# Performance work log

Hardware: AMD Instinct MI355X
Metric: run time of the kernel (lower is better)

Reference implementation:

```python
import jax, jax.numpy as jnp
import numpy as np

N_GENE, N_PATH, N_VACC = 50000, 20000, 10000
N_TOT = N_GENE + N_PATH + N_VACC
HID = 128
E_PER = 250000
K_APPNP = 8
ALPHA = 0.1
N_LAYERS = 2


def setup_inputs() -> dict:
    key = jax.random.key(0)
    ks = iter(jax.random.split(key, 40))
    f32 = jnp.float32

    def nrm(shape, scale=1.0):
        return jax.random.normal(next(ks), shape, dtype=f32) * scale

    def edges(n_src, n_dst):
        src = jax.random.randint(next(ks), (E_PER,), 0, n_src)
        dst = jax.random.randint(next(ks), (E_PER,), 0, n_dst)
        return jnp.stack([src, dst]).astype(jnp.int32)

    return {
        "x_gene": nrm((N_GENE, 256)),
        "x_pathway": nrm((N_PATH, 128)),
        "x_vaccine": nrm((N_VACC, 64)),
        "win_gene": nrm((HID, 256), 256 ** -0.5),
        "bin_gene": jnp.zeros((HID,), f32),
        "win_pathway": nrm((HID, 128), 128 ** -0.5),
        "bin_pathway": jnp.zeros((HID,), f32),
        "win_vaccine": nrm((HID, 64), 64 ** -0.5),
        "bin_vaccine": jnp.zeros((HID,), f32),
        "w_sage_l": nrm((N_LAYERS, 4, HID, HID), HID ** -0.5),
        "b_sage_l": jnp.zeros((N_LAYERS, 4, HID), f32),
        "w_sage_r": nrm((N_LAYERS, 4, HID, HID), HID ** -0.5),
        "ei_targets": edges(N_VACC, N_GENE),    # vaccine -> gene
        "ei_in": edges(N_GENE, N_PATH),         # gene -> pathway
        "ei_contains": edges(N_PATH, N_GENE),   # pathway -> gene
        "ei_interacts": edges(N_GENE, N_GENE),  # gene -> gene
    }


def _sage(x_src, x_dst, ei, wl, bl, wr, n_dst):
    # PyG SAGEConv(aggr='mean'): lin_l(mean_j x_src[j]) + lin_r(x_dst); bias lives in lin_l
    src, dst = ei[0], ei[1]
    s = jax.ops.segment_sum(x_src[src], dst, num_segments=n_dst)
    cnt = jax.ops.segment_sum(jnp.ones((ei.shape[1],), x_src.dtype), dst, num_segments=n_dst)
    agg = s / jnp.maximum(cnt, 1.0)[:, None]  # isolated dst nodes -> 0
    return agg @ wl.T + bl + x_dst @ wr.T


def _forward(x_gene, x_pathway, x_vaccine, win_gene, bin_gene, win_pathway, bin_pathway,
             win_vaccine, bin_vaccine, w_sage_l, b_sage_l, w_sage_r,
             ei_targets, ei_in, ei_contains, ei_interacts):
    # input projections + relu
    hg = jax.nn.relu(x_gene @ win_gene.T + bin_gene)
    hp = jax.nn.relu(x_pathway @ win_pathway.T + bin_pathway)
    hv = jax.nn.relu(x_vaccine @ win_vaccine.T + bin_vaccine)
    # hetero SAGE layers with residual + relu (dropout: eval mode -> identity)
    for l in range(N_LAYERS):
        o_tg = _sage(hv, hg, ei_targets, w_sage_l[l, 0], b_sage_l[l, 0], w_sage_r[l, 0], N_GENE)
        o_in = _sage(hg, hp, ei_in, w_sage_l[l, 1], b_sage_l[l, 1], w_sage_r[l, 1], N_PATH)
        o_ct = _sage(hp, hg, ei_contains, w_sage_l[l, 2], b_sage_l[l, 2], w_sage_r[l, 2], N_GENE)
        o_ii = _sage(hg, hg, ei_interacts, w_sage_l[l, 3], b_sage_l[l, 3], w_sage_r[l, 3], N_GENE)
        hg = jax.nn.relu(hg + (o_tg + o_ct + o_ii) / 3.0)  # HeteroConv aggr='mean' over 3 relations
        hp = jax.nn.relu(hp + o_in)
        hv = jax.nn.relu(hv)  # no incoming relation -> zero message
    # APPNP on homogeneous graph; node order = [gene | pathway | vaccine]
    OG, OP, OV = 0, N_GENE, N_GENE + N_PATH
    loops = jnp.arange(N_TOT, dtype=jnp.int32)
    row = jnp.concatenate([ei_targets[0] + OV, ei_in[0] + OG, ei_contains[0] + OP, ei_interacts[0] + OG, loops])
    col = jnp.concatenate([ei_targets[1] + OG, ei_in[1] + OP, ei_contains[1] + OG, ei_interacts[1] + OG, loops])
    deg = jax.ops.segment_sum(jnp.ones(row.shape, hg.dtype), col, num_segments=N_TOT)
    dinv = jnp.where(deg > 0, deg ** -0.5, 0.0)
    norm = (dinv[row] * dinv[col])[:, None]
    h0 = jnp.concatenate([hg, hp, hv], axis=0)  # [N_TOT, HID]

    def step(z, _):
        m = jax.ops.segment_sum(norm * z[row], col, num_segments=N_TOT)
        return (1.0 - ALPHA) * m + ALPHA * h0, None

    z, _ = jax.lax.scan(step, h0, None, length=K_APPNP)
    return z  # [N_TOT, HID]; rows 0:50000 gene, 50000:70000 pathway, 70000:80000 vaccine


def reference(x_gene, x_pathway, x_vaccine, win_gene, bin_gene, win_pathway, bin_pathway,
              win_vaccine, bin_vaccine, w_sage_l, b_sage_l, w_sage_r,
              ei_targets, ei_in, ei_contains, ei_interacts):
    return _forward(x_gene, x_pathway, x_vaccine, win_gene, bin_gene, win_pathway, bin_pathway,
                    win_vaccine, bin_vaccine, w_sage_l, b_sage_l, w_sage_r,
                    ei_targets, ei_in, ei_contains, ei_interacts)
```

## Files before the change

### kernel.cpp

```cpp
#include <hip/hip_runtime.h>

#define N_GENE 50000
#define N_PATH 20000
#define N_VACC 10000
#define N_TOT  80000
#define HID    128
#define E_PER  250000
#define OG 0
#define OP 50000
#define OV 70000

typedef __bf16    bf16x8 __attribute__((ext_vector_type(8)));
typedef __bf16    bf16x4 __attribute__((ext_vector_type(4)));
typedef _Float16  f16x4  __attribute__((ext_vector_type(4)));
typedef float     f32x4  __attribute__((ext_vector_type(4)));

__constant__ int c_segn[4] = {N_GENE, N_PATH, N_GENE, N_GENE};
__constant__ int c_segb[4] = {0, 50000, 70000, 120000};
#define CNT_TOTAL 170000

struct Off4 { int* p[4]; };
struct CntSeg { const int* dst; int* cnt; };
struct Cnt4 { CntSeg s[4]; };
struct F4Seg { const int* ei; const int* off; int* rows; int2* pk; int soff; };
struct F4 { F4Seg s[4]; };
struct AggSeg { const int* rows; const int* off; __bf16* out; int ldo; int n; };
struct Agg4 { AggSeg s[4]; };
struct CsrP { const int* off; const int2* pk; };


__global__ void count4_kernel(Cnt4 a, int* __restrict__ rank)
{
    int seg = blockIdx.y;
    int e = blockIdx.x * 256 + threadIdx.x;
    if (e < E_PER) rank[seg * E_PER + e] = atomicAdd(&a.s[seg].cnt[a.s[seg].dst[e]], 1);
}

__global__ void scan1_kernel(const int* __restrict__ cnt, int* __restrict__ partials)
{
    int seg = blockIdx.y, blk = blockIdx.x;
    int n = c_segn[seg];
    if (blk >= ((n + 4095) >> 12)) return;
    const int* base = cnt + c_segb[seg];
    int t = threadIdx.x;
    int i0 = (blk << 12) + t * 16;
    int s = 0;
#pragma unroll
    for (int j = 0; j < 16; j++) { int i = i0 + j; if (i < n) s += base[i]; }
    __shared__ int sh[256];
    sh[t] = s; __syncthreads();
    for (int d = 128; d; d >>= 1) { if (t < d) sh[t] += sh[t + d]; __syncthreads(); }
    if (t == 0) partials[seg * 32 + blk] = sh[0];
}

__global__ void scan2_kernel(int* __restrict__ partials, Off4 offs)
{
    int s = threadIdx.x;
    if (s < 4) {
        int n = c_segn[s];
        int nb = (n + 4095) >> 12;
        int run = 0;
        for (int b = 0; b < nb; b++) { int v = partials[s * 32 + b]; partials[s * 32 + b] = run; run += v; }
        offs.p[s][n] = run;
    }
}

__global__ void scan3_kernel(const int* __restrict__ cnt, const int* __restrict__ partials, Off4 offs)
{
    int seg = blockIdx.y, blk = blockIdx.x;
    int n = c_segn[seg];
    if (blk >= ((n + 4095) >> 12)) return;
    const int* base = cnt + c_segb[seg];
    int* off = offs.p[seg];
    int t = threadIdx.x;
    int i0 = (blk << 12) + t * 16;
    int loc[16];
    int s = 0;
#pragma unroll
    for (int j = 0; j < 16; j++) { int i = i0 + j; int v = (i < n) ? base[i] : 0; loc[j] = s; s += v; }
    __shared__ int sh[256];
    sh[t] = s; __syncthreads();
    for (int d = 1; d < 256; d <<= 1) {
        int v = (t >= d) ? sh[t - d] : 0; __syncthreads();
        sh[t] += v; __syncthreads();
    }
    int base_off = sh[t] - s + partials[seg * 32 + blk];
#pragma unroll
    for (int j = 0; j < 16; j++) { int i = i0 + j; if (i < n) off[i] = base_off + loc[j]; }
}

__global__ void dinv_kernel(const int* __restrict__ r0, const int* __restrict__ r1,
                            const int* __restrict__ r2, const int* __restrict__ r3,
                            float* __restrict__ dinv)
{
    int i = blockIdx.x * 256 + threadIdx.x;
    if (i >= N_TOT) return;
    int deg = 1;
    if (i < N_GENE) deg += (r0[i + 1] - r0[i]) + (r2[i + 1] - r2[i]) + (r3[i + 1] - r3[i]);
    else if (i < OV) { int k = i - OP; deg += r1[k + 1] - r1[k]; }
    dinv[i] = rsqrtf((float)deg);
}

__global__ void fill4_kernel(F4 a, const int* __restrict__ rank, const float* __restrict__ dinv)
{
    int seg = blockIdx.y;
    int e = blockIdx.x * 256 + threadIdx.x;
    if (e >= E_PER) return;
    const int* ei = a.s[seg].ei;
    int s = ei[e] + a.s[seg].soff;
    int d = ei[E_PER + e];
    int pos = a.s[seg].off[d] + rank[seg * E_PER + e];
    a.s[seg].rows[pos] = s;
    if (a.s[seg].pk) a.s[seg].pk[pos] = make_int2(s, __float_as_int(dinv[s]));
}


__global__ void agg_all_kernel(Agg4 a, const __bf16* __restrict__ Hbf)
{
    int seg = blockIdx.y;
    int t = threadIdx.x;
    int node = blockIdx.x * 8 + (t >> 5);
    if (node >= a.s[seg].n) return;
    const int* rows = a.s[seg].rows;
    int sub = t & 31;
    int s = a.s[seg].off[node], e = a.s[seg].off[node + 1];
    f32x4 A0 = {0,0,0,0}, A1 = {0,0,0,0}, A2v = {0,0,0,0}, A3 = {0,0,0,0};
    int i = s;
    for (; i + 4 <= e; i += 4) {
        int r0 = rows[i], r1 = rows[i + 1], r2 = rows[i + 2], r3 = rows[i + 3];
        bf16x4 x0 = *(const bf16x4*)&Hbf[(size_t)r0 * HID + sub * 4];
        bf16x4 x1 = *(const bf16x4*)&Hbf[(size_t)r1 * HID + sub * 4];
        bf16x4 x2 = *(const bf16x4*)&Hbf[(size_t)r2 * HID + sub * 4];
        bf16x4 x3 = *(const bf16x4*)&Hbf[(size_t)r3 * HID + sub * 4];
#pragma unroll
        for (int j = 0; j < 4; j++) {
            A0[j] += (float)x0[j]; A1[j] += (float)x1[j];
            A2v[j] += (float)x2[j]; A3[j] += (float)x3[j];
        }
    }
    for (; i < e; i++) {
        bf16x4 x = *(const bf16x4*)&Hbf[(size_t)rows[i] * HID + sub * 4];
#pragma unroll
        for (int j = 0; j < 4; j++) A0[j] += (float)x[j];
    }
    f32x4 acc = (A0 + A1) + (A2v + A3);
    float inv = (e > s) ? 1.0f / (float)(e - s) : 0.0f;
    bf16x4 o;
    o[0] = (__bf16)(acc[0] * inv); o[1] = (__bf16)(acc[1] * inv);
    o[2] = (__bf16)(acc[2] * inv); o[3] = (__bf16)(acc[3] * inv);
    *(bf16x4*)&a.s[seg].out[(size_t)node * a.s[seg].ldo + sub * 4] = o;
}

__global__ void base_kernel(const float* __restrict__ H, const int* __restrict__ r0rows,
                            const int* __restrict__ r0off, const float* __restrict__ dinv,
                            _Float16* __restrict__ base, _Float16* __restrict__ z0,
                            float* __restrict__ dout)
{
    int t = threadIdx.x;
    int node = blockIdx.x * 8 + (t >> 5);
    int sub = t & 31;
    size_t idx = (size_t)node * HID + sub * 4;
    f32x4 h = *(const f32x4*)&H[idx];
    if (node >= OV) { *(f32x4*)&dout[idx] = h; return; }
    f32x4 acc = {0.f, 0.f, 0.f, 0.f};
    if (node < N_GENE) {
        for (int i = r0off[node]; i < r0off[node + 1]; i++) {
            acc += *(const f32x4*)&H[(size_t)r0rows[i] * HID + sub * 4];
        }
        acc *= 0.9f * dinv[node];
    }
    f32x4 b = h * 0.1f + acc;
    f16x4 bo, z;
    bo[0] = (_Float16)b[0]; bo[1] = (_Float16)b[1]; bo[2] = (_Float16)b[2]; bo[3] = (_Float16)b[3];
    z[0] = (_Float16)h[0]; z[1] = (_Float16)h[1]; z[2] = (_Float16)h[2]; z[3] = (_Float16)h[3];
    *(f16x4*)&base[idx] = bo;
    *(f16x4*)&z0[idx] = z;
}

__device__ __forceinline__ void gathp(const int* __restrict__ off, const int2* __restrict__ pk,
                                      int node, int sub, const _Float16* __restrict__ zin,
                                      f32x4& A0, f32x4& A1, f32x4& A2v, f32x4& A3)
{
    int s = off[node], e = off[node + 1];
    int i = s;
    for (; i + 4 <= e; i += 4) {
        int2 p0 = pk[i], p1 = pk[i + 1], p2 = pk[i + 2], p3 = pk[i + 3];
        f16x4 x0 = *(const f16x4*)&zin[(size_t)p0.x * HID + sub * 4];
        f16x4 x1 = *(const f16x4*)&zin[(size_t)p1.x * HID + sub * 4];
        f16x4 x2 = *(const f16x4*)&zin[(size_t)p2.x * HID + sub * 4];
        f16x4 x3 = *(const f16x4*)&zin[(size_t)p3.x * HID + sub * 4];
        float w0 = __int_as_float(p0.y), w1 = __int_as_float(p1.y);
        float w2 = __int_as_float(p2.y), w3 = __int_as_float(p3.y);
#pragma unroll
        for (int j = 0; j < 4; j++) {
            A0[j] += (float)x0[j] * w0; A1[j] += (float)x1[j] * w1;
            A2v[j] += (float)x2[j] * w2; A3[j] += (float)x3[j] * w3;
        }
    }
    for (; i < e; i++) {
        int2 p = pk[i];
        float w = __int_as_float(p.y);
        f16x4 x = *(const f16x4*)&zin[(size_t)p.x * HID + sub * 4];
#pragma unroll
        for (int j = 0; j < 4; j++) A0[j] += (float)x[j] * w;
    }
}

template<typename OT>
__launch_bounds__(256)
__global__ void appnp_kernel(const _Float16* __restrict__ zin, OT* __restrict__ zout,
                             const _Float16* __restrict__ base,
                             CsrP c1, CsrP c2, CsrP c3, const float* __restrict__ dinv)
{
    int t = threadIdx.x;
    int c = blockIdx.x * 8 + (t >> 5);
    int sub = t & 31;
    f32x4 A0 = {0,0,0,0}, A1 = {0,0,0,0}, A2v = {0,0,0,0}, A3 = {0,0,0,0};
    if (c < OP) {
        gathp(c2.off, c2.pk, c, sub, zin, A0, A1, A2v, A3);
        gathp(c3.off, c3.pk, c, sub, zin, A0, A1, A2v, A3);
    } else {
        gathp(c1.off, c1.pk, c - OP, sub, zin, A0, A1, A2v, A3);
    }
    f32x4 acc = (A0 + A1) + (A2v + A3);
    float dc = dinv[c];
    size_t idx = (size_t)c * HID + sub * 4;
    f16x4 zi = *(const f16x4*)&zin[idx];
    f16x4 bs = *(const f16x4*)&base[idx];
    f32x4 res;
    float d2 = dc * dc;
#pragma unroll
    for (int j = 0; j < 4; j++) res[j] = 0.9f * (dc * acc[j] + d2 * (float)zi[j]) + (float)bs[j];
    if constexpr (sizeof(OT) == 2) {
        f16x4 o;
        o[0] = (_Float16)res[0]; o[1] = (_Float16)res[1]; o[2] = (_Float16)res[2]; o[3] = (_Float16)res[3];
        *(f16x4*)&zout[idx] = o;
    } else {
        *(f32x4*)&zout[idx] = res;
    }
}


__global__ void prep_all_kernel(const float* __restrict__ wg, const float* __restrict__ wp,
                                const float* __restrict__ wv,
                                __bf16* __restrict__ obg, __bf16* __restrict__ obp, __bf16* __restrict__ obv,
                                const float* __restrict__ wsl, const float* __restrict__ bsl,
                                const float* __restrict__ wsr,
                                __bf16* __restrict__ Wg0, __bf16* __restrict__ Wg1,
                                __bf16* __restrict__ Wp0, __bf16* __restrict__ Wp1,
                                float* __restrict__ bg0, float* __restrict__ bg1,
                                float* __restrict__ bp0, float* __restrict__ bp1)
{
    int y = blockIdx.y;
    int i = blockIdx.x * 256 + threadIdx.x;
    if (y == 0) {
        if (i < 32768) obg[i] = (__bf16)wg[i];
        if (i < 16384) obp[i] = (__bf16)wp[i];
        if (i < 8192)  obv[i] = (__bf16)wv[i];
        return;
    }
    int layer = y - 1;
    const float* WL = wsl + (size_t)layer * 4 * HID * HID;
    const float* WR = wsr + (size_t)layer * 4 * HID * HID;
    __bf16* Wg = layer ? Wg1 : Wg0;
    __bf16* Wp = layer ? Wp1 : Wp0;
    float* bg = layer ? bg1 : bg0;
    float* bp = layer ? bp1 : bp0;
    if (i < 128 * 512) {
        int nr = i >> 9, k = i & 511;
        float v;
        if (k < 128)      v = WL[0 * 16384 + nr * 128 + k];
        else if (k < 256) v = WL[2 * 16384 + nr * 128 + (k - 128)];
        else if (k < 384) v = WL[3 * 16384 + nr * 128 + (k - 256)];
        else {
            int kk = k - 384;
            v = WR[0 * 16384 + nr * 128 + kk] + WR[2 * 16384 + nr * 128 + kk] + WR[3 * 16384 + nr * 128 + kk];
        }
        Wg[i] = (__bf16)v;
    }
    if (i < 128 * 256) {
        int nr = i >> 8, k = i & 255;
        float v = (k < 128) ? WL[1 * 16384 + nr * 128 + k] : WR[1 * 16384 + nr * 128 + (k - 128)];
        Wp[i] = (__bf16)v;
    }
    if (i < 128) {
        const float* BL = bsl + (size_t)layer * 4 * HID;
        bg[i] = BL[0 * 128 + i] + BL[2 * 128 + i] + BL[3 * 128 + i];
        bp[i] = BL[1 * 128 + i];
    }
}


struct GemmSeg {
    int blk0, M, KT, K1;
    const void* A1; const __bf16* A2;
    const __bf16* W; const float* bias;
    float scale;
    float* H; __bf16* Hbf;
    int a_f32, sage;
};
template<int NSEG> struct GemmSegs { GemmSeg s[NSEG]; };

template<int NSEG>
__launch_bounds__(256)
__global__ void tgemm_multi(GemmSegs<NSEG> segs)
{
    int si = 0;
#pragma unroll
    for (int k = 1; k < NSEG; k++) if ((int)blockIdx.x >= segs.s[k].blk0) si = k;
    GemmSeg sg = segs.s[si];

    __shared__ __bf16 lds[128 * 40];
    int t = threadIdx.x;
    int wave = t >> 6, lane = t & 63;
    int r = lane & 15, quad = lane >> 4;
    int mbase = (blockIdx.x - sg.blk0) * 128 + wave * 32;
    int M = sg.M, KT = sg.KT, K1 = sg.K1;
    int mm0 = min(mbase + r, M - 1);
    int mm1 = min(mbase + 16 + r, M - 1);
    const float* Af = (const float*)sg.A1;
    const __bf16* Ab = (const __bf16*)sg.A1;

    f32x4 acc[2][8];
#pragma unroll
    for (int s = 0; s < 2; s++)
#pragma unroll
        for (int n = 0; n < 8; n++) acc[s][n] = (f32x4){0.f, 0.f, 0.f, 0.f};

    int srow = t >> 1;
    int selt = (t & 1) * 16;

    for (int k0 = 0; k0 < KT; k0 += 32) {
        __syncthreads();
        {
            const __bf16* wsrc = sg.W + (size_t)srow * KT + k0 + selt;
            bf16x8 w0 = *(const bf16x8*)wsrc;
            bf16x8 w1 = *(const bf16x8*)(wsrc + 8);
            *(bf16x8*)&lds[srow * 40 + selt] = w0;
            *(bf16x8*)&lds[srow * 40 + selt + 8] = w1;
        }
        bf16x8 a0, a1;
        if (sg.a_f32) {
            const float* p0 = Af + (size_t)mm0 * KT + k0 + quad * 8;
            const float* p1 = Af + (size_t)mm1 * KT + k0 + quad * 8;
            f32x4 x0 = *(const f32x4*)p0, x1 = *(const f32x4*)(p0 + 4);
            f32x4 y0 = *(const f32x4*)p1, y1 = *(const f32x4*)(p1 + 4);
#pragma unroll
            for (int j = 0; j < 4; j++) { a0[j] = (__bf16)x0[j]; a0[j + 4] = (__bf16)x1[j]; }
#pragma unroll
            for (int j = 0; j < 4; j++) { a1[j] = (__bf16)y0[j]; a1[j + 4] = (__bf16)y1[j]; }
        } else if (k0 < K1) {
            a0 = *(const bf16x8*)(Ab + (size_t)mm0 * K1 + k0 + quad * 8);
            a1 = *(const bf16x8*)(Ab + (size_t)mm1 * K1 + k0 + quad * 8);
        } else {
            a0 = *(const bf16x8*)(sg.A2 + (size_t)mm0 * 128 + (k0 - K1) + quad * 8);
            a1 = *(const bf16x8*)(sg.A2 + (size_t)mm1 * 128 + (k0 - K1) + quad * 8);
        }
        __syncthreads();
#pragma unroll
        for (int nt = 0; nt < 8; nt++) {
            bf16x8 b = *(const bf16x8*)&lds[(nt * 16 + r) * 40 + quad * 8];
            acc[0][nt] = __builtin_amdgcn_mfma_f32_16x16x32_bf16(a0, b, acc[0][nt], 0, 0, 0);
            acc[1][nt] = __builtin_amdgcn_mfma_f32_16x16x32_bf16(a1, b, acc[1][nt], 0, 0, 0);
        }
    }

#pragma unroll
    for (int sub = 0; sub < 2; sub++) {
#pragma unroll
        for (int nt = 0; nt < 8; nt++) {
            int n = nt * 16 + r;
            float bv = sg.bias[n];
#pragma unroll
            for (int i = 0; i < 4; i++) {
                int row = mbase + sub * 16 + quad * 4 + i;
                if (row >= M) continue;
                size_t idx = (size_t)row * HID + n;
                float v;
                if (sg.sage) v = fmaxf(sg.H[idx] + (acc[sub][nt][i] + bv) * sg.scale, 0.f);
                else         v = fmaxf(acc[sub][nt][i] + bv, 0.f);
                sg.H[idx] = v;
                sg.Hbf[idx] = (__bf16)v;
            }
        }
    }
}


extern "C" void kernel_launch(void* const* d_in, const int* in_sizes, int n_in,
                              void* d_out, int out_size, void* d_ws, size_t ws_size,
                              hipStream_t stream)
{
    (void)in_sizes; (void)n_in; (void)out_size; (void)ws_size;

    const float* x_gene = (const float*)d_in[0];
    const float* x_path = (const float*)d_in[1];
    const float* x_vacc = (const float*)d_in[2];
    const float* win_g  = (const float*)d_in[3];
    const float* bin_g  = (const float*)d_in[4];
    const float* win_p  = (const float*)d_in[5];
    const float* bin_p  = (const float*)d_in[6];
    const float* win_v  = (const float*)d_in[7];
    const float* bin_v  = (const float*)d_in[8];
    const float* wsl    = (const float*)d_in[9];
    const float* bsl    = (const float*)d_in[10];
    const float* wsr    = (const float*)d_in[11];
    const int* ei_tg  = (const int*)d_in[12];
    const int* ei_ing = (const int*)d_in[13];
    const int* ei_ct  = (const int*)d_in[14];
    const int* ei_ii  = (const int*)d_in[15];

    char* p = (char*)d_ws;
    auto alloc = [&](size_t b) { char* r = p; p += (b + 255) & ~((size_t)255); return r; };

    float*    H    = (float*)alloc((size_t)N_TOT * HID * 4);
    _Float16* BASE = (_Float16*)alloc((size_t)OV * HID * 2);
    __bf16*   Hbf  = (__bf16*)alloc((size_t)N_TOT * HID * 2);
    _Float16* Z1   = (_Float16*)alloc((size_t)OV * HID * 2);
    _Float16* Z2   = (_Float16*)alloc((size_t)OV * HID * 2);
    __bf16* AGG_G = (__bf16*)alloc((size_t)N_GENE * 384 * 2);
    __bf16* AGG_P = (__bf16*)alloc((size_t)N_PATH * 128 * 2);
    float* dinv   = (float*)alloc((size_t)N_TOT * 4);
    int* r_rows[4], *r_off[4];
    for (int r = 0; r < 4; r++) r_rows[r] = (int*)alloc((size_t)E_PER * 4);
    r_off[0] = (int*)alloc((size_t)(N_GENE + 1) * 4);
    r_off[1] = (int*)alloc((size_t)(N_PATH + 1) * 4);
    r_off[2] = (int*)alloc((size_t)(N_GENE + 1) * 4);
    r_off[3] = (int*)alloc((size_t)(N_GENE + 1) * 4);
    int2* pk1 = (int2*)alloc((size_t)E_PER * 8);
    int2* pk2 = (int2*)alloc((size_t)E_PER * 8);
    int2* pk3 = (int2*)alloc((size_t)E_PER * 8);
    int* rank = (int*)alloc((size_t)4 * E_PER * 4);
    int* partials = (int*)alloc((size_t)4 * 32 * 4);
    __bf16* wbf_g = (__bf16*)alloc((size_t)HID * 256 * 2);
    __bf16* wbf_p = (__bf16*)alloc((size_t)HID * 128 * 2);
    __bf16* wbf_v = (__bf16*)alloc((size_t)HID * 64 * 2);
    __bf16* Wg[2]; __bf16* Wp[2]; float* bg[2]; float* bp[2];
    for (int l = 0; l < 2; l++) {
        Wg[l] = (__bf16*)alloc((size_t)128 * 512 * 2);
        Wp[l] = (__bf16*)alloc((size_t)128 * 256 * 2);
        bg[l] = (float*)alloc(128 * 4);
        bp[l] = (float*)alloc(128 * 4);
    }
    char* zb = p;
    int* cnt = (int*)alloc((size_t)CNT_TOTAL * 4);
    hipMemsetAsync(zb, 0, (size_t)(p - zb), stream);

    Off4 offs;
    offs.p[0] = r_off[0]; offs.p[1] = r_off[1]; offs.p[2] = r_off[2]; offs.p[3] = r_off[3];

    const int GE = (E_PER + 255) / 256;
    const int TB_G = (N_GENE + 127) / 128;
    const int TB_P = (N_PATH + 127) / 128;
    const int TB_V = (N_VACC + 127) / 128;

    prep_all_kernel<<<dim3(256, 3), 256, 0, stream>>>(win_g, win_p, win_v, wbf_g, wbf_p, wbf_v,
                                                      wsl, bsl, wsr, Wg[0], Wg[1], Wp[0], Wp[1],
                                                      bg[0], bg[1], bp[0], bp[1]);

    Cnt4 c4;
    c4.s[0] = {ei_tg + E_PER,  cnt + 0};
    c4.s[1] = {ei_ing + E_PER, cnt + 50000};
    c4.s[2] = {ei_ct + E_PER,  cnt + 70000};
    c4.s[3] = {ei_ii + E_PER,  cnt + 120000};
    count4_kernel<<<dim3(GE, 4), 256, 0, stream>>>(c4, rank);

    dim3 sg((N_GENE + 4095) / 4096, 4);
    scan1_kernel<<<sg, 256, 0, stream>>>(cnt, partials);
    scan2_kernel<<<1, 64, 0, stream>>>(partials, offs);
    scan3_kernel<<<sg, 256, 0, stream>>>(cnt, partials, offs);

    dinv_kernel<<<(N_TOT + 255) / 256, 256, 0, stream>>>(r_off[0], r_off[1], r_off[2], r_off[3], dinv);

    F4 f4;
    f4.s[0] = {ei_tg,  r_off[0], r_rows[0], nullptr, OV};
    f4.s[1] = {ei_ing, r_off[1], r_rows[1], pk1,     OG};
    f4.s[2] = {ei_ct,  r_off[2], r_rows[2], pk2,     OP};
    f4.s[3] = {ei_ii,  r_off[3], r_rows[3], pk3,     OG};
    fill4_kernel<<<dim3(GE, 4), 256, 0, stream>>>(f4, rank, dinv);

    GemmSegs<3> gp;
    gp.s[0] = {0,           N_GENE, 256, 256, x_gene, nullptr, wbf_g, bin_g, 1.f, H, Hbf, 1, 0};
    gp.s[1] = {TB_G,        N_PATH, 128, 128, x_path, nullptr, wbf_p, bin_p, 1.f,
               H + (size_t)OP * HID, Hbf + (size_t)OP * HID, 1, 0};
    gp.s[2] = {TB_G + TB_P, N_VACC,  64,  64, x_vacc, nullptr, wbf_v, bin_v, 1.f,
               H + (size_t)OV * HID, Hbf + (size_t)OV * HID, 1, 0};
    tgemm_multi<3><<<TB_G + TB_P + TB_V, 256, 0, stream>>>(gp);

    for (int l = 0; l < 2; l++) {
        Agg4 ag;
        ag.s[0] = {r_rows[0], r_off[0], AGG_G + 0,   384, N_GENE};
        ag.s[1] = {r_rows[2], r_off[2], AGG_G + 128, 384, N_GENE};
        ag.s[2] = {r_rows[3], r_off[3], AGG_G + 256, 384, N_GENE};
        ag.s[3] = {r_rows[1], r_off[1], AGG_P,       128, N_PATH};
        agg_all_kernel<<<dim3(N_GENE / 8, 4), 256, 0, stream>>>(ag, Hbf);

        GemmSegs<2> gs;
        gs.s[0] = {0,    N_GENE, 512, 384, AGG_G, Hbf, Wg[l], bg[l], 1.0f / 3.0f, H, Hbf, 0, 1};
        gs.s[1] = {TB_G, N_PATH, 256, 128, AGG_P, Hbf + (size_t)OP * HID, Wp[l], bp[l], 1.0f,
                   H + (size_t)OP * HID, Hbf + (size_t)OP * HID, 0, 1};
        tgemm_multi<2><<<TB_G + TB_P, 256, 0, stream>>>(gs);
    }

    float* dout = (float*)d_out;
    base_kernel<<<N_TOT / 8, 256, 0, stream>>>(H, r_rows[0], r_off[0], dinv, BASE, Z1, dout);

    CsrP c1 = {r_off[1], pk1};
    CsrP c2 = {r_off[2], pk2};
    CsrP c3 = {r_off[3], pk3};
    const int GA = OV / 8;
    appnp_kernel<<<GA, 256, 0, stream>>>(Z1, Z2, BASE, c1, c2, c3, dinv);
    appnp_kernel<<<GA, 256, 0, stream>>>(Z2, Z1, BASE, c1, c2, c3, dinv);
    appnp_kernel<<<GA, 256, 0, stream>>>(Z1, Z2, BASE, c1, c2, c3, dinv);
    appnp_kernel<<<GA, 256, 0, stream>>>(Z2, Z1, BASE, c1, c2, c3, dinv);
    appnp_kernel<<<GA, 256, 0, stream>>>(Z1, Z2, BASE, c1, c2, c3, dinv);
    appnp_kernel<<<GA, 256, 0, stream>>>(Z2, Z1, BASE, c1, c2, c3, dinv);
    appnp_kernel<<<GA, 256, 0, stream>>>(Z1, Z2, BASE, c1, c2, c3, dinv);
    appnp_kernel<<<GA, 256, 0, stream>>>(Z2, dout, BASE, c1, c2, c3, dinv);
}
```

Baseline: 791.6 us.

## Keep hidden state only in fp16 and widen gathers to 16-byte loads

```diff
diff --git a/kernel.cpp b/kernel.cpp
--- a/kernel.cpp
+++ b/kernel.cpp
@@ -10,8 +10,7 @@
 #define OP 50000
 #define OV 70000
 
-typedef __bf16    bf16x8 __attribute__((ext_vector_type(8)));
-typedef __bf16    bf16x4 __attribute__((ext_vector_type(4)));
+typedef _Float16  f16x8  __attribute__((ext_vector_type(8)));
 typedef _Float16  f16x4  __attribute__((ext_vector_type(4)));
 typedef float     f32x4  __attribute__((ext_vector_type(4)));
 
@@ -24,7 +23,7 @@
 struct Cnt4 { CntSeg s[4]; };
 struct F4Seg { const int* ei; const int* off; int* rows; int2* pk; int soff; };
 struct F4 { F4Seg s[4]; };
-struct AggSeg { const int* rows; const int* off; __bf16* out; int ldo; int n; };
+struct AggSeg { const int* rows; const int* off; _Float16* out; int ldo; int n; };
 struct Agg4 { AggSeg s[4]; };
 struct CsrP { const int* off; const int2* pk; };
 
@@ -115,94 +114,103 @@
 }
 
 
-__global__ void agg_all_kernel(Agg4 a, const __bf16* __restrict__ Hbf)
+__global__ void agg_all_kernel(Agg4 a, const _Float16* __restrict__ Hh)
 {
     int seg = blockIdx.y;
     int t = threadIdx.x;
-    int node = blockIdx.x * 8 + (t >> 5);
+    int node = blockIdx.x * 16 + (t >> 4);
     if (node >= a.s[seg].n) return;
     const int* rows = a.s[seg].rows;
-    int sub = t & 31;
+    int sub = t & 15;
     int s = a.s[seg].off[node], e = a.s[seg].off[node + 1];
-    f32x4 A0 = {0,0,0,0}, A1 = {0,0,0,0}, A2v = {0,0,0,0}, A3 = {0,0,0,0};
+    float acc0[8] = {}, acc1[8] = {};
     int i = s;
     for (; i + 4 <= e; i += 4) {
         int r0 = rows[i], r1 = rows[i + 1], r2 = rows[i + 2], r3 = rows[i + 3];
-        bf16x4 x0 = *(const bf16x4*)&Hbf[(size_t)r0 * HID + sub * 4];
-        bf16x4 x1 = *(const bf16x4*)&Hbf[(size_t)r1 * HID + sub * 4];
-        bf16x4 x2 = *(const bf16x4*)&Hbf[(size_t)r2 * HID + sub * 4];
-        bf16x4 x3 = *(const bf16x4*)&Hbf[(size_t)r3 * HID + sub * 4];
-#pragma unroll
-        for (int j = 0; j < 4; j++) {
-            A0[j] += (float)x0[j]; A1[j] += (float)x1[j];
-            A2v[j] += (float)x2[j]; A3[j] += (float)x3[j];
+        f16x8 x0 = *(const f16x8*)&Hh[(size_t)r0 * HID + sub * 8];
+        f16x8 x1 = *(const f16x8*)&Hh[(size_t)r1 * HID + sub * 8];
+        f16x8 x2 = *(const f16x8*)&Hh[(size_t)r2 * HID + sub * 8];
+        f16x8 x3 = *(const f16x8*)&Hh[(size_t)r3 * HID + sub * 8];
+#pragma unroll
+        for (int j = 0; j < 8; j++) {
+            acc0[j] += (float)x0[j] + (float)x1[j];
+            acc1[j] += (float)x2[j] + (float)x3[j];
         }
     }
     for (; i < e; i++) {
-        bf16x4 x = *(const bf16x4*)&Hbf[(size_t)rows[i] * HID + sub * 4];
-#pragma unroll
-        for (int j = 0; j < 4; j++) A0[j] += (float)x[j];
-    }
-    f32x4 acc = (A0 + A1) + (A2v + A3);
+        f16x8 x = *(const f16x8*)&Hh[(size_t)rows[i] * HID + sub * 8];
+#pragma unroll
+        for (int j = 0; j < 8; j++) acc0[j] += (float)x[j];
+    }
     float inv = (e > s) ? 1.0f / (float)(e - s) : 0.0f;
-    bf16x4 o;
-    o[0] = (__bf16)(acc[0] * inv); o[1] = (__bf16)(acc[1] * inv);
-    o[2] = (__bf16)(acc[2] * inv); o[3] = (__bf16)(acc[3] * inv);
-    *(bf16x4*)&a.s[seg].out[(size_t)node * a.s[seg].ldo + sub * 4] = o;
-}
-
-__global__ void base_kernel(const float* __restrict__ H, const int* __restrict__ r0rows,
+    f16x8 o;
+#pragma unroll
+    for (int j = 0; j < 8; j++) o[j] = (_Float16)((acc0[j] + acc1[j]) * inv);
+    *(f16x8*)&a.s[seg].out[(size_t)node * a.s[seg].ldo + sub * 8] = o;
+}
+
+__global__ void base_kernel(const _Float16* __restrict__ Hh, const int* __restrict__ r0rows,
                             const int* __restrict__ r0off, const float* __restrict__ dinv,
                             _Float16* __restrict__ base, _Float16* __restrict__ z0,
                             float* __restrict__ dout)
 {
     int t = threadIdx.x;
-    int node = blockIdx.x * 8 + (t >> 5);
-    int sub = t & 31;
-    size_t idx = (size_t)node * HID + sub * 4;
-    f32x4 h = *(const f32x4*)&H[idx];
-    if (node >= OV) { *(f32x4*)&dout[idx] = h; return; }
-    f32x4 acc = {0.f, 0.f, 0.f, 0.f};
+    int node = blockIdx.x * 16 + (t >> 4);
+    int sub = t & 15;
+    size_t idx = (size_t)node * HID + sub * 8;
+    f16x8 h = *(const f16x8*)&Hh[idx];
+    if (node >= OV) {
+        f32x4 o0, o1;
+#pragma unroll
+        for (int j = 0; j < 4; j++) { o0[j] = (float)h[j]; o1[j] = (float)h[j + 4]; }
+        *(f32x4*)&dout[idx] = o0;
+        *(f32x4*)&dout[idx + 4] = o1;
+        return;
+    }
+    float acc[8] = {};
     if (node < N_GENE) {
         for (int i = r0off[node]; i < r0off[node + 1]; i++) {
-            acc += *(const f32x4*)&H[(size_t)r0rows[i] * HID + sub * 4];
-        }
-        acc *= 0.9f * dinv[node];
-    }
-    f32x4 b = h * 0.1f + acc;
-    f16x4 bo, z;
-    bo[0] = (_Float16)b[0]; bo[1] = (_Float16)b[1]; bo[2] = (_Float16)b[2]; bo[3] = (_Float16)b[3];
-    z[0] = (_Float16)h[0]; z[1] = (_Float16)h[1]; z[2] = (_Float16)h[2]; z[3] = (_Float16)h[3];
-    *(f16x4*)&base[idx] = bo;
-    *(f16x4*)&z0[idx] = z;
+            f16x8 v = *(const f16x8*)&Hh[(size_t)r0rows[i] * HID + sub * 8];
+#pragma unroll
+            for (int j = 0; j < 8; j++) acc[j] += (float)v[j];
+        }
+        float sc = 0.9f * dinv[node];
+#pragma unroll
+        for (int j = 0; j < 8; j++) acc[j] *= sc;
+    }
+    f16x8 bo;
+#pragma unroll
+    for (int j = 0; j < 8; j++) bo[j] = (_Float16)(0.1f * (float)h[j] + acc[j]);
+    *(f16x8*)&base[idx] = bo;
+    *(f16x8*)&z0[idx] = h;
 }
 
 __device__ __forceinline__ void gathp(const int* __restrict__ off, const int2* __restrict__ pk,
                                       int node, int sub, const _Float16* __restrict__ zin,
-                                      f32x4& A0, f32x4& A1, f32x4& A2v, f32x4& A3)
+                                      float (&A0)[8], float (&A1)[8])
 {
     int s = off[node], e = off[node + 1];
     int i = s;
     for (; i + 4 <= e; i += 4) {
         int2 p0 = pk[i], p1 = pk[i + 1], p2 = pk[i + 2], p3 = pk[i + 3];
-        f16x4 x0 = *(const f16x4*)&zin[(size_t)p0.x * HID + sub * 4];
-        f16x4 x1 = *(const f16x4*)&zin[(size_t)p1.x * HID + sub * 4];
-        f16x4 x2 = *(const f16x4*)&zin[(size_t)p2.x * HID + sub * 4];
-        f16x4 x3 = *(const f16x4*)&zin[(size_t)p3.x * HID + sub * 4];
+        f16x8 x0 = *(const f16x8*)&zin[(size_t)p0.x * HID + sub * 8];
+        f16x8 x1 = *(const f16x8*)&zin[(size_t)p1.x * HID + sub * 8];
+        f16x8 x2 = *(const f16x8*)&zin[(size_t)p2.x * HID + sub * 8];
+        f16x8 x3 = *(const f16x8*)&zin[(size_t)p3.x * HID + sub * 8];
         float w0 = __int_as_float(p0.y), w1 = __int_as_float(p1.y);
         float w2 = __int_as_float(p2.y), w3 = __int_as_float(p3.y);
 #pragma unroll
-        for (int j = 0; j < 4; j++) {
-            A0[j] += (float)x0[j] * w0; A1[j] += (float)x1[j] * w1;
-            A2v[j] += (float)x2[j] * w2; A3[j] += (float)x3[j] * w3;
+        for (int j = 0; j < 8; j++) {
+            A0[j] += (float)x0[j] * w0 + (float)x1[j] * w1;
+            A1[j] += (float)x2[j] * w2 + (float)x3[j] * w3;
         }
     }
     for (; i < e; i++) {
         int2 p = pk[i];
         float w = __int_as_float(p.y);
-        f16x4 x = *(const f16x4*)&zin[(size_t)p.x * HID + sub * 4];
-#pragma unroll
-        for (int j = 0; j < 4; j++) A0[j] += (float)x[j] * w;
+        f16x8 x = *(const f16x8*)&zin[(size_t)p.x * HID + sub * 8];
+#pragma unroll
+        for (int j = 0; j < 8; j++) A0[j] += (float)x[j] * w;
     }
 }
 
@@ -213,57 +221,62 @@
                              CsrP c1, CsrP c2, CsrP c3, const float* __restrict__ dinv)
 {
     int t = threadIdx.x;
-    int c = blockIdx.x * 8 + (t >> 5);
-    int sub = t & 31;
-    f32x4 A0 = {0,0,0,0}, A1 = {0,0,0,0}, A2v = {0,0,0,0}, A3 = {0,0,0,0};
+    int c = blockIdx.x * 16 + (t >> 4);
+    int sub = t & 15;
+    float A0[8] = {}, A1[8] = {};
     if (c < OP) {
-        gathp(c2.off, c2.pk, c, sub, zin, A0, A1, A2v, A3);
-        gathp(c3.off, c3.pk, c, sub, zin, A0, A1, A2v, A3);
+        gathp(c2.off, c2.pk, c, sub, zin, A0, A1);
+        gathp(c3.off, c3.pk, c, sub, zin, A0, A1);
     } else {
-        gathp(c1.off, c1.pk, c - OP, sub, zin, A0, A1, A2v, A3);
-    }
-    f32x4 acc = (A0 + A1) + (A2v + A3);
+        gathp(c1.off, c1.pk, c - OP, sub, zin, A0, A1);
+    }
     float dc = dinv[c];
-    size_t idx = (size_t)c * HID + sub * 4;
-    f16x4 zi = *(const f16x4*)&zin[idx];
-    f16x4 bs = *(const f16x4*)&base[idx];
-    f32x4 res;
     float d2 = dc * dc;
-#pragma unroll
-    for (int j = 0; j < 4; j++) res[j] = 0.9f * (dc * acc[j] + d2 * (float)zi[j]) + (float)bs[j];
+    size_t idx = (size_t)c * HID + sub * 8;
+    f16x8 zi = *(const f16x8*)&zin[idx];
+    f16x8 bs = *(const f16x8*)&base[idx];
+    float res[8];
+#pragma unroll
+    for (int j = 0; j < 8; j++)
+        res[j] = 0.9f * (dc * (A0[j] + A1[j]) + d2 * (float)zi[j]) + (float)bs[j];
     if constexpr (sizeof(OT) == 2) {
-        f16x4 o;
-        o[0] = (_Float16)res[0]; o[1] = (_Float16)res[1]; o[2] = (_Float16)res[2]; o[3] = (_Float16)res[3];
-        *(f16x4*)&zout[idx] = o;
+        f16x8 o;
+#pragma unroll
+        for (int j = 0; j < 8; j++) o[j] = (_Float16)res[j];
+        *(f16x8*)&zout[idx] = o;
     } else {
-        *(f32x4*)&zout[idx] = res;
+        f32x4 o0, o1;
+#pragma unroll
+        for (int j = 0; j < 4; j++) { o0[j] = res[j]; o1[j] = res[j + 4]; }
+        *(f32x4*)&zout[idx] = o0;
+        *(f32x4*)&zout[idx + 4] = o1;
     }
 }
 
 
 __global__ void prep_all_kernel(const float* __restrict__ wg, const float* __restrict__ wp,
                                 const float* __restrict__ wv,
-                                __bf16* __restrict__ obg, __bf16* __restrict__ obp, __bf16* __restrict__ obv,
+                                _Float16* __restrict__ obg, _Float16* __restrict__ obp, _Float16* __restrict__ obv,
                                 const float* __restrict__ wsl, const float* __restrict__ bsl,
                                 const float* __restrict__ wsr,
-                                __bf16* __restrict__ Wg0, __bf16* __restrict__ Wg1,
-                                __bf16* __restrict__ Wp0, __bf16* __restrict__ Wp1,
+                                _Float16* __restrict__ Wg0, _Float16* __restrict__ Wg1,
+                                _Float16* __restrict__ Wp0, _Float16* __restrict__ Wp1,
                                 float* __restrict__ bg0, float* __restrict__ bg1,
                                 float* __restrict__ bp0, float* __restrict__ bp1)
 {
     int y = blockIdx.y;
     int i = blockIdx.x * 256 + threadIdx.x;
     if (y == 0) {
-        if (i < 32768) obg[i] = (__bf16)wg[i];
-        if (i < 16384) obp[i] = (__bf16)wp[i];
-        if (i < 8192)  obv[i] = (__bf16)wv[i];
+        if (i < 32768) obg[i] = (_Float16)wg[i];
+        if (i < 16384) obp[i] = (_Float16)wp[i];
+        if (i < 8192)  obv[i] = (_Float16)wv[i];
         return;
     }
     int layer = y - 1;
     const float* WL = wsl + (size_t)layer * 4 * HID * HID;
     const float* WR = wsr + (size_t)layer * 4 * HID * HID;
-    __bf16* Wg = layer ? Wg1 : Wg0;
-    __bf16* Wp = layer ? Wp1 : Wp0;
+    _Float16* Wg = layer ? Wg1 : Wg0;
+    _Float16* Wp = layer ? Wp1 : Wp0;
     float* bg = layer ? bg1 : bg0;
     float* bp = layer ? bp1 : bp0;
     if (i < 128 * 512) {
@@ -276,12 +289,12 @@
             int kk = k - 384;
             v = WR[0 * 16384 + nr * 128 + kk] + WR[2 * 16384 + nr * 128 + kk] + WR[3 * 16384 + nr * 128 + kk];
         }
-        Wg[i] = (__bf16)v;
+        Wg[i] = (_Float16)v;
     }
     if (i < 128 * 256) {
         int nr = i >> 8, k = i & 255;
         float v = (k < 128) ? WL[1 * 16384 + nr * 128 + k] : WR[1 * 16384 + nr * 128 + (k - 128)];
-        Wp[i] = (__bf16)v;
+        Wp[i] = (_Float16)v;
     }
     if (i < 128) {
         const float* BL = bsl + (size_t)layer * 4 * HID;
@@ -291,35 +304,21 @@
 }
 
 
-struct GemmSeg {
-    int blk0, M, KT, K1;
-    const void* A1; const __bf16* A2;
-    const __bf16* W; const float* bias;
-    float scale;
-    float* H; __bf16* Hbf;
-    int a_f32, sage;
-};
-template<int NSEG> struct GemmSegs { GemmSeg s[NSEG]; };
-
-template<int NSEG>
+template<int KT, int K1, bool A_F32, bool SAGE>
 __launch_bounds__(256)
-__global__ void tgemm_multi(GemmSegs<NSEG> segs)
-{
-    int si = 0;
-#pragma unroll
-    for (int k = 1; k < NSEG; k++) if ((int)blockIdx.x >= segs.s[k].blk0) si = k;
-    GemmSeg sg = segs.s[si];
-
-    __shared__ __bf16 lds[128 * 40];
+__global__ void tgemm_kernel(const void* __restrict__ A1_, const _Float16* __restrict__ A2,
+                             const _Float16* __restrict__ W, const float* __restrict__ bias,
+                             float scale, _Float16* __restrict__ Hh, int M)
+{
+    __shared__ _Float16 lds[128 * 40];
     int t = threadIdx.x;
     int wave = t >> 6, lane = t & 63;
     int r = lane & 15, quad = lane >> 4;
-    int mbase = (blockIdx.x - sg.blk0) * 128 + wave * 32;
-    int M = sg.M, KT = sg.KT, K1 = sg.K1;
+    int mbase = blockIdx.x * 128 + wave * 32;
     int mm0 = min(mbase + r, M - 1);
     int mm1 = min(mbase + 16 + r, M - 1);
-    const float* Af = (const float*)sg.A1;
-    const __bf16* Ab = (const __bf16*)sg.A1;
+    const float* Af = (const float*)A1_;
+    const _Float16* Ab = (const _Float16*)A1_;
 
     f32x4 acc[2][8];
 #pragma unroll
@@ -330,38 +329,39 @@
     int srow = t >> 1;
     int selt = (t & 1) * 16;
 
+#pragma unroll
     for (int k0 = 0; k0 < KT; k0 += 32) {
         __syncthreads();
         {
-            const __bf16* wsrc = sg.W + (size_t)srow * KT + k0 + selt;
-            bf16x8 w0 = *(const bf16x8*)wsrc;
-            bf16x8 w1 = *(const bf16x8*)(wsrc + 8);
-            *(bf16x8*)&lds[srow * 40 + selt] = w0;
-            *(bf16x8*)&lds[srow * 40 + selt + 8] = w1;
-        }
-        bf16x8 a0, a1;
-        if (sg.a_f32) {
+            const _Float16* wsrc = W + (size_t)srow * KT + k0 + selt;
+            f16x8 w0 = *(const f16x8*)wsrc;
+            f16x8 w1 = *(const f16x8*)(wsrc + 8);
+            *(f16x8*)&lds[srow * 40 + selt] = w0;
+            *(f16x8*)&lds[srow * 40 + selt + 8] = w1;
+        }
+        f16x8 a0, a1;
+        if constexpr (A_F32) {
             const float* p0 = Af + (size_t)mm0 * KT + k0 + quad * 8;
             const float* p1 = Af + (size_t)mm1 * KT + k0 + quad * 8;
             f32x4 x0 = *(const f32x4*)p0, x1 = *(const f32x4*)(p0 + 4);
             f32x4 y0 = *(const f32x4*)p1, y1 = *(const f32x4*)(p1 + 4);
 #pragma unroll
-            for (int j = 0; j < 4; j++) { a0[j] = (__bf16)x0[j]; a0[j + 4] = (__bf16)x1[j]; }
-#pragma unroll
-            for (int j = 0; j < 4; j++) { a1[j] = (__bf16)y0[j]; a1[j + 4] = (__bf16)y1[j]; }
+            for (int j = 0; j < 4; j++) { a0[j] = (_Float16)x0[j]; a0[j + 4] = (_Float16)x1[j]; }
+#pragma unroll
+            for (int j = 0; j < 4; j++) { a1[j] = (_Float16)y0[j]; a1[j + 4] = (_Float16)y1[j]; }
         } else if (k0 < K1) {
-            a0 = *(const bf16x8*)(Ab + (size_t)mm0 * K1 + k0 + quad * 8);
-            a1 = *(const bf16x8*)(Ab + (size_t)mm1 * K1 + k0 + quad * 8);
+            a0 = *(const f16x8*)(Ab + (size_t)mm0 * K1 + k0 + quad * 8);
+            a1 = *(const f16x8*)(Ab + (size_t)mm1 * K1 + k0 + quad * 8);
         } else {
-            a0 = *(const bf16x8*)(sg.A2 + (size_t)mm0 * 128 + (k0 - K1) + quad * 8);
-            a1 = *(const bf16x8*)(sg.A2 + (size_t)mm1 * 128 + (k0 - K1) + quad * 8);
+            a0 = *(const f16x8*)(A2 + (size_t)mm0 * 128 + (k0 - K1) + quad * 8);
+            a1 = *(const f16x8*)(A2 + (size_t)mm1 * 128 + (k0 - K1) + quad * 8);
         }
         __syncthreads();
 #pragma unroll
         for (int nt = 0; nt < 8; nt++) {
-            bf16x8 b = *(const bf16x8*)&lds[(nt * 16 + r) * 40 + quad * 8];
-            acc[0][nt] = __builtin_amdgcn_mfma_f32_16x16x32_bf16(a0, b, acc[0][nt], 0, 0, 0);
-            acc[1][nt] = __builtin_amdgcn_mfma_f32_16x16x32_bf16(a1, b, acc[1][nt], 0, 0, 0);
+            f16x8 b = *(const f16x8*)&lds[(nt * 16 + r) * 40 + quad * 8];
+            acc[0][nt] = __builtin_amdgcn_mfma_f32_16x16x32_f16(a0, b, acc[0][nt], 0, 0, 0);
+            acc[1][nt] = __builtin_amdgcn_mfma_f32_16x16x32_f16(a1, b, acc[1][nt], 0, 0, 0);
         }
     }
 
@@ -370,17 +370,16 @@
 #pragma unroll
         for (int nt = 0; nt < 8; nt++) {
             int n = nt * 16 + r;
-            float bv = sg.bias[n];
+            float bv = bias[n];
 #pragma unroll
             for (int i = 0; i < 4; i++) {
                 int row = mbase + sub * 16 + quad * 4 + i;
                 if (row >= M) continue;
                 size_t idx = (size_t)row * HID + n;
                 float v;
-                if (sg.sage) v = fmaxf(sg.H[idx] + (acc[sub][nt][i] + bv) * sg.scale, 0.f);
-                else         v = fmaxf(acc[sub][nt][i] + bv, 0.f);
-                sg.H[idx] = v;
-                sg.Hbf[idx] = (__bf16)v;
+                if constexpr (SAGE) v = fmaxf((float)Hh[idx] + (acc[sub][nt][i] + bv) * scale, 0.f);
+                else                v = fmaxf(acc[sub][nt][i] + bv, 0.f);
+                Hh[idx] = (_Float16)v;
             }
         }
     }
@@ -413,13 +412,12 @@
     char* p = (char*)d_ws;
     auto alloc = [&](size_t b) { char* r = p; p += (b + 255) & ~((size_t)255); return r; };
 
-    float*    H    = (float*)alloc((size_t)N_TOT * HID * 4);
+    _Float16* Hh   = (_Float16*)alloc((size_t)N_TOT * HID * 2);
     _Float16* BASE = (_Float16*)alloc((size_t)OV * HID * 2);
-    __bf16*   Hbf  = (__bf16*)alloc((size_t)N_TOT * HID * 2);
     _Float16* Z1   = (_Float16*)alloc((size_t)OV * HID * 2);
     _Float16* Z2   = (_Float16*)alloc((size_t)OV * HID * 2);
-    __bf16* AGG_G = (__bf16*)alloc((size_t)N_GENE * 384 * 2);
-    __bf16* AGG_P = (__bf16*)alloc((size_t)N_PATH * 128 * 2);
+    _Float16* AGG_G = (_Float16*)alloc((size_t)N_GENE * 384 * 2);
+    _Float16* AGG_P = (_Float16*)alloc((size_t)N_PATH * 128 * 2);
     float* dinv   = (float*)alloc((size_t)N_TOT * 4);
     int* r_rows[4], *r_off[4];
     for (int r = 0; r < 4; r++) r_rows[r] = (int*)alloc((size_t)E_PER * 4);
@@ -432,13 +430,13 @@
     int2* pk3 = (int2*)alloc((size_t)E_PER * 8);
     int* rank = (int*)alloc((size_t)4 * E_PER * 4);
     int* partials = (int*)alloc((size_t)4 * 32 * 4);
-    __bf16* wbf_g = (__bf16*)alloc((size_t)HID * 256 * 2);
-    __bf16* wbf_p = (__bf16*)alloc((size_t)HID * 128 * 2);
-    __bf16* wbf_v = (__bf16*)alloc((size_t)HID * 64 * 2);
-    __bf16* Wg[2]; __bf16* Wp[2]; float* bg[2]; float* bp[2];
+    _Float16* wh_g = (_Float16*)alloc((size_t)HID * 256 * 2);
+    _Float16* wh_p = (_Float16*)alloc((size_t)HID * 128 * 2);
+    _Float16* wh_v = (_Float16*)alloc((size_t)HID * 64 * 2);
+    _Float16* Wg[2]; _Float16* Wp[2]; float* bg[2]; float* bp[2];
     for (int l = 0; l < 2; l++) {
-        Wg[l] = (__bf16*)alloc((size_t)128 * 512 * 2);
-        Wp[l] = (__bf16*)alloc((size_t)128 * 256 * 2);
+        Wg[l] = (_Float16*)alloc((size_t)128 * 512 * 2);
+        Wp[l] = (_Float16*)alloc((size_t)128 * 256 * 2);
         bg[l] = (float*)alloc(128 * 4);
         bp[l] = (float*)alloc(128 * 4);
     }
@@ -454,7 +452,7 @@
     const int TB_P = (N_PATH + 127) / 128;
     const int TB_V = (N_VACC + 127) / 128;
 
-    prep_all_kernel<<<dim3(256, 3), 256, 0, stream>>>(win_g, win_p, win_v, wbf_g, wbf_p, wbf_v,
+    prep_all_kernel<<<dim3(256, 3), 256, 0, stream>>>(win_g, win_p, win_v, wh_g, wh_p, wh_v,
                                                       wsl, bsl, wsr, Wg[0], Wg[1], Wp[0], Wp[1],
                                                       bg[0], bg[1], bp[0], bp[1]);
 
@@ -479,13 +477,11 @@
     f4.s[3] = {ei_ii,  r_off[3], r_rows[3], pk3,     OG};
     fill4_kernel<<<dim3(GE, 4), 256, 0, stream>>>(f4, rank, dinv);
 
-    GemmSegs<3> gp;
-    gp.s[0] = {0,           N_GENE, 256, 256, x_gene, nullptr, wbf_g, bin_g, 1.f, H, Hbf, 1, 0};
-    gp.s[1] = {TB_G,        N_PATH, 128, 128, x_path, nullptr, wbf_p, bin_p, 1.f,
-               H + (size_t)OP * HID, Hbf + (size_t)OP * HID, 1, 0};
-    gp.s[2] = {TB_G + TB_P, N_VACC,  64,  64, x_vacc, nullptr, wbf_v, bin_v, 1.f,
-               H + (size_t)OV * HID, Hbf + (size_t)OV * HID, 1, 0};
-    tgemm_multi<3><<<TB_G + TB_P + TB_V, 256, 0, stream>>>(gp);
+    tgemm_kernel<256, 256, true, false><<<TB_G, 256, 0, stream>>>(x_gene, nullptr, wh_g, bin_g, 1.f, Hh, N_GENE);
+    tgemm_kernel<128, 128, true, false><<<TB_P, 256, 0, stream>>>(x_path, nullptr, wh_p, bin_p, 1.f,
+                                                                  Hh + (size_t)OP * HID, N_PATH);
+    tgemm_kernel< 64,  64, true, false><<<TB_V, 256, 0, stream>>>(x_vacc, nullptr, wh_v, bin_v, 1.f,
+                                                                  Hh + (size_t)OV * HID, N_VACC);
 
     for (int l = 0; l < 2; l++) {
         Agg4 ag;
@@ -493,22 +489,21 @@
         ag.s[1] = {r_rows[2], r_off[2], AGG_G + 128, 384, N_GENE};
         ag.s[2] = {r_rows[3], r_off[3], AGG_G + 256, 384, N_GENE};
         ag.s[3] = {r_rows[1], r_off[1], AGG_P,       128, N_PATH};
-        agg_all_kernel<<<dim3(N_GENE / 8, 4), 256, 0, stream>>>(ag, Hbf);
-
-        GemmSegs<2> gs;
-        gs.s[0] = {0,    N_GENE, 512, 384, AGG_G, Hbf, Wg[l], bg[l], 1.0f / 3.0f, H, Hbf, 0, 1};
-        gs.s[1] = {TB_G, N_PATH, 256, 128, AGG_P, Hbf + (size_t)OP * HID, Wp[l], bp[l], 1.0f,
-                   H + (size_t)OP * HID, Hbf + (size_t)OP * HID, 0, 1};
-        tgemm_multi<2><<<TB_G + TB_P, 256, 0, stream>>>(gs);
+        agg_all_kernel<<<dim3((N_GENE + 15) / 16, 4), 256, 0, stream>>>(ag, Hh);
+
+        tgemm_kernel<512, 384, false, true><<<TB_G, 256, 0, stream>>>(AGG_G, Hh, Wg[l], bg[l],
+                                                                      1.0f / 3.0f, Hh, N_GENE);
+        tgemm_kernel<256, 128, false, true><<<TB_P, 256, 0, stream>>>(AGG_P, Hh + (size_t)OP * HID, Wp[l], bp[l],
+                                                                      1.0f, Hh + (size_t)OP * HID, N_PATH);
     }
 
     float* dout = (float*)d_out;
-    base_kernel<<<N_TOT / 8, 256, 0, stream>>>(H, r_rows[0], r_off[0], dinv, BASE, Z1, dout);
+    base_kernel<<<N_TOT / 16, 256, 0, stream>>>(Hh, r_rows[0], r_off[0], dinv, BASE, Z1, dout);
 
     CsrP c1 = {r_off[1], pk1};
     CsrP c2 = {r_off[2], pk2};
     CsrP c3 = {r_off[3], pk3};
-    const int GA = OV / 8;
+    const int GA = OV / 16;
     appnp_kernel<<<GA, 256, 0, stream>>>(Z1, Z2, BASE, c1, c2, c3, dinv);
     appnp_kernel<<<GA, 256, 0, stream>>>(Z2, Z1, BASE, c1, c2, c3, dinv);
     appnp_kernel<<<GA, 256, 0, stream>>>(Z1, Z2, BASE, c1, c2, c3, dinv);
```

New measurement: 722.5 us. 1.1x faster.
